# Kernel optimization log

Hardware: AMD Instinct MI355X
Metric: run time of the kernel (lower is better)

Reference implementation:

```python
import jax, jax.numpy as jnp
import numpy as np

S = 2048        # tokens (single prefill sequence)
HID = 3584      # hidden_size
H = 16          # num query heads
KV = 8          # num kv heads
D = 256         # head_dim
WINDOW = 1024   # sliding window size
CAP = 50.0      # logit softcap
SCALE = 256.0 ** -0.5   # query_pre_attn_scalar ** -0.5
THETA = 10000.0


def setup_inputs() -> dict:
    key = jax.random.key(0)
    ks = jax.random.split(key, 5)
    hidden_states = jax.random.normal(ks[0], (S, HID), dtype=jnp.float32)
    positions = jnp.arange(S, dtype=jnp.int32)
    Wq = jax.random.normal(ks[1], (HID, H * D), dtype=jnp.float32) * 0.02
    Wk = jax.random.normal(ks[2], (HID, KV * D), dtype=jnp.float32) * 0.02
    Wv = jax.random.normal(ks[3], (HID, KV * D), dtype=jnp.float32) * 0.02
    Wo = jax.random.normal(ks[4], (H * D, HID), dtype=jnp.float32) * 0.02
    return {"hidden_states": hidden_states, "positions": positions,
            "Wq": Wq, "Wk": Wk, "Wv": Wv, "Wo": Wo}


def _rope_neox(x, positions):
    # x: [S, n_heads, D]; neox-style: rotate halves, full rotary_dim == D
    half = D // 2
    inv_freq = 1.0 / (THETA ** (jnp.arange(0, half, dtype=jnp.float32) * 2.0 / D))
    freqs = positions.astype(jnp.float32)[:, None] * inv_freq[None, :]  # [S, half]
    cos = jnp.cos(freqs)[:, None, :].astype(x.dtype)
    sin = jnp.sin(freqs)[:, None, :].astype(x.dtype)
    x1, x2 = x[..., :half], x[..., half:]
    return jnp.concatenate([x1 * cos - x2 * sin, x2 * cos + x1 * sin], axis=-1)


def reference(hidden_states, positions, Wq, Wk, Wv, Wo):
    # QKV projections (no bias)
    q = (hidden_states @ Wq).reshape(S, H, D)
    k = (hidden_states @ Wk).reshape(S, KV, D)
    v = (hidden_states @ Wv).reshape(S, KV, D)
    q = _rope_neox(q, positions)
    k = _rope_neox(k, positions)
    # grouped-query attention: G query heads per kv head
    G = H // KV
    qg = q.reshape(S, KV, G, D)
    scores = jnp.einsum('qkgd,skd->kgqs', qg, k) * jnp.asarray(SCALE, q.dtype)
    # logit soft-capping
    scores = CAP * jnp.tanh(scores / CAP)
    # causal + sliding-window mask
    i = positions[:, None]
    j = positions[None, :]
    mask = (j <= i) & ((i - j) < WINDOW)   # [S, S]
    neg = jnp.finfo(scores.dtype).min
    scores = jnp.where(mask[None, None, :, :], scores, neg)
    p = jax.nn.softmax(scores, axis=-1)
    attn = jnp.einsum('kgqs,skd->qkgd', p, v).reshape(S, H * D)
    return attn @ Wo
```

## Files before the change

### kernel.cpp

```cpp
#include <hip/hip_runtime.h>
#include <stdint.h>

#define S 2048
#define HID 3584
#define NH 16
#define NKV 8
#define DH 256
#define WINDOW 1024
#define SCALE 0.0625f
#define CAP 50.0f

typedef short s16x8 __attribute__((ext_vector_type(8)));
typedef float f32x4 __attribute__((ext_vector_type(4)));

__device__ __forceinline__ short f2bf(float f) {
  union { float f; uint32_t u; } c; c.f = f;
  uint32_t u = c.u;
  uint32_t r = (u + 0x7FFFu + ((u >> 16) & 1u)) >> 16;
  return (short)r;
}
__device__ __forceinline__ float bf2f(short s) {
  union { uint32_t u; float f; } c;
  c.u = ((uint32_t)(uint16_t)s) << 16;
  return c.f;
}
__device__ __forceinline__ void gll16(const void* g, void* l) {
  __builtin_amdgcn_global_load_lds((const __attribute__((address_space(1))) void*)g,
                                   (__attribute__((address_space(3))) void*)l, 16, 0, 0);
}

__global__ void rope_table_kernel(float2* __restrict__ tbl) {
  int idx = blockIdx.x * 256 + threadIdx.x;
  int s = idx >> 7, i = idx & 127;
  float inv = __expf(-(float)i * (9.210340371976184f / 128.0f));
  float fr = (float)s * inv;
  tbl[idx] = make_float2(cosf(fr), sinf(fr));
}

__global__ void conv_hs_kernel(const float* __restrict__ src, short* __restrict__ dst) {
  int gid = blockIdx.x * 256 + threadIdx.x;
  float4 a = *(const float4*)&src[(size_t)gid * 8];
  float4 b = *(const float4*)&src[(size_t)gid * 8 + 4];
  s16x8 o;
  o[0] = f2bf(a.x); o[1] = f2bf(a.y); o[2] = f2bf(a.z); o[3] = f2bf(a.w);
  o[4] = f2bf(b.x); o[5] = f2bf(b.y); o[6] = f2bf(b.z); o[7] = f2bf(b.w);
  *(s16x8*)&dst[(size_t)gid * 8] = o;
}

__global__ __launch_bounds__(256)
void transpose_all_kernel(const float* __restrict__ Wq, const float* __restrict__ Wk,
                          const float* __restrict__ Wv, const float* __restrict__ Wo,
                          short* __restrict__ Wt, short* __restrict__ WtO)
{
  __shared__ __align__(16) short t[64][76];
  int b = blockIdx.x;
  const float* src; short* dst; int K, N, lb;
  if (b < 3584)      { src = Wq; dst = Wt;                       K = HID;  N = 4096; lb = b; }
  else if (b < 5376) { src = Wk; dst = Wt + (size_t)4096 * HID;  K = HID;  N = 2048; lb = b - 3584; }
  else if (b < 7168) { src = Wv; dst = Wt + (size_t)6144 * HID;  K = HID;  N = 2048; lb = b - 5376; }
  else               { src = Wo; dst = WtO;                      K = 4096; N = HID;  lb = b - 7168; }
  int ntn = N >> 6;
  int tn = lb % ntn, tk = lb / ntn;
  int tid = threadIdx.x;
  int c = tid & 63, rg = tid >> 6;
  #pragma unroll
  for (int i = 0; i < 4; ++i) {
    int r0 = i * 16 + rg * 4;
    short tmp[4];
    #pragma unroll
    for (int j = 0; j < 4; ++j)
      tmp[j] = f2bf(src[(size_t)(tk * 64 + r0 + j) * N + tn * 64 + c]);
    *(short4*)&t[c][r0] = *(short4*)tmp;
  }
  __syncthreads();
  #pragma unroll
  for (int it = 0; it < 2; ++it) {
    int flat = it * 256 + tid;
    int n = flat >> 3, kc = flat & 7;
    *(s16x8*)&dst[(size_t)(tn * 64 + n) * K + tk * 64 + kc * 8] = *(s16x8*)&t[n][kc * 8];
  }
}

__global__ __launch_bounds__(256)
void transpose_v_kernel(const short* __restrict__ vsb, short* __restrict__ vtb)
{
  __shared__ short t[64][74];
  int b = blockIdx.x;
  int kv = b >> 7;
  int rem = b & 127;
  int s0 = (rem >> 2) * 64, d0 = (rem & 3) * 64;
  const short* src = vsb + ((size_t)kv * S + s0) * DH + d0;
  short* dst = vtb + ((size_t)kv * DH + d0) * S + s0;
  int tid = threadIdx.x;
  int c = tid & 63, sb = (tid >> 6) * 16;
  #pragma unroll
  for (int ss = 0; ss < 16; ++ss)
    t[c][sb + ss] = src[(size_t)(sb + ss) * DH + c];
  __syncthreads();
  #pragma unroll
  for (int it = 0; it < 2; ++it) {
    int flat = it * 256 + tid;
    int r = flat >> 3, cc = (flat & 7) * 8;
    *(s16x8*)&dst[(size_t)r * S + cc] = *(s16x8*)&t[r][cc];
  }
}

__global__ __launch_bounds__(256, 2)
void qkv_gemm_kernel(const short* __restrict__ hsb, const short* __restrict__ Wt,
                     short* __restrict__ qb, short* __restrict__ kbuf,
                     short* __restrict__ vsb)
{
  __shared__ __align__(16) short Asb[256 * 64];
  __shared__ __align__(16) short Bsb[128 * 64];
  int bid = blockIdx.x;
  int i = bid >> 3;
  int bm = i & 7;
  int bn = (bid & 7) * 8 + (i >> 3);
  int m0 = bm * 256, n0 = bn * 128;
  int tid = threadIdx.x, w = tid >> 6, lane = tid & 63;
  int lr = lane & 15, lk = lane >> 4;
  int wm = (w >> 1) * 128, wn = (w & 1) * 64;
  int r7 = lr & 7;
  int abase = (wm + lr) * 64 + ((lk ^ r7) * 8);
  int bbase = (wn + lr) * 64 + ((lk ^ r7) * 8);
  int row8 = tid >> 3;
  int colsw = ((tid & 7) ^ (row8 & 7)) * 8;
  const short* srcA = hsb + (size_t)(m0 + row8) * HID + colsw;
  const short* srcB = Wt + (size_t)(n0 + row8) * HID + colsw;
  f32x4 acc[8][4] = {};
  for (int t = 0; t < HID / 64; ++t) {
    const short* sa = srcA + t * 64;
    const short* sb = srcB + t * 64;
    #pragma unroll
    for (int r = 0; r < 8; ++r)
      gll16(sa + (size_t)(r * 32) * HID, Asb + r * 2048 + w * 512);
    #pragma unroll
    for (int r = 0; r < 4; ++r)
      gll16(sb + (size_t)(r * 32) * HID, Bsb + r * 2048 + w * 512);
    __syncthreads();
    s16x8 bf[4][2];
    #pragma unroll
    for (int nf = 0; nf < 4; ++nf)
      #pragma unroll
      for (int kh = 0; kh < 2; ++kh)
        bf[nf][kh] = *(const s16x8*)&Bsb[(bbase + nf * 16 * 64) ^ (kh * 32)];
    #pragma unroll
    for (int mh = 0; mh < 2; ++mh) {
      s16x8 af[4][2];
      #pragma unroll
      for (int mf = 0; mf < 4; ++mf)
        #pragma unroll
        for (int kh = 0; kh < 2; ++kh)
          af[mf][kh] = *(const s16x8*)&Asb[(abase + (mh * 64 + mf * 16) * 64) ^ (kh * 32)];
      __builtin_amdgcn_s_setprio(1);
      #pragma unroll
      for (int mf = 0; mf < 4; ++mf)
        #pragma unroll
        for (int nf = 0; nf < 4; ++nf) {
          acc[mh * 4 + mf][nf] = __builtin_amdgcn_mfma_f32_16x16x32_bf16(
              af[mf][0], bf[nf][0], acc[mh * 4 + mf][nf], 0, 0, 0);
          acc[mh * 4 + mf][nf] = __builtin_amdgcn_mfma_f32_16x16x32_bf16(
              af[mf][1], bf[nf][1], acc[mh * 4 + mf][nf], 0, 0, 0);
        }
      __builtin_amdgcn_s_setprio(0);
    }
    __syncthreads();
  }
  int region = (n0 < 4096) ? 0 : ((n0 < 6144) ? 1 : 2);
  #pragma unroll
  for (int m = 0; m < 8; ++m) {
    int srow_b = m0 + wm + m * 16 + lk * 4;
    #pragma unroll
    for (int n = 0; n < 4; ++n) {
      int ncol = n0 + wn + n * 16 + lr;
      #pragma unroll
      for (int r = 0; r < 4; ++r) {
        int srow = srow_b + r;
        short bv = f2bf(acc[m][n][r]);
        if (region == 0) {
          int h = ncol >> 8, d = ncol & 255;
          qb[((size_t)h * S + srow) * DH + d] = bv;
        } else if (region == 1) {
          int c = ncol - 4096; int kv = c >> 8, d = c & 255;
          kbuf[((size_t)kv * S + srow) * DH + d] = bv;
        } else {
          int c = ncol - 6144; int kv = c >> 8, d = c & 255;
          vsb[((size_t)kv * S + srow) * DH + d] = bv;
        }
      }
    }
  }
}

__global__ __launch_bounds__(256)
void out_gemm_kernel(const short* __restrict__ attnb, const short* __restrict__ WtO,
                     float* __restrict__ out)
{
  __shared__ __align__(16) short Asb[128 * 64];
  __shared__ __align__(16) short Bsb[128 * 64];
  int bid = blockIdx.x;
  int flat = (bid & 7) * 56 + (bid >> 3);
  int bn = flat >> 4, bm = flat & 15;
  int m0 = bm * 128, n0 = bn * 128;
  int tid = threadIdx.x, w = tid >> 6, lane = tid & 63;
  int lr = lane & 15, lk = lane >> 4;
  int wm = (w >> 1) * 64, wn = (w & 1) * 64;
  int r7 = lr & 7;
  int abase = (wm + lr) * 64 + ((lk ^ r7) * 8);
  int bbase = (wn + lr) * 64 + ((lk ^ r7) * 8);
  int row8 = tid >> 3;
  int colsw = ((tid & 7) ^ (row8 & 7)) * 8;
  const short* srcA = attnb + (size_t)(m0 + row8) * 4096 + colsw;
  const short* srcB = WtO + (size_t)(n0 + row8) * 4096 + colsw;
  f32x4 acc[4][4] = {};
  for (int t = 0; t < 4096 / 64; ++t) {
    const short* sa = srcA + t * 64;
    const short* sb = srcB + t * 64;
    #pragma unroll
    for (int r = 0; r < 4; ++r)
      gll16(sa + (size_t)(r * 32) * 4096, Asb + r * 2048 + w * 512);
    #pragma unroll
    for (int r = 0; r < 4; ++r)
      gll16(sb + (size_t)(r * 32) * 4096, Bsb + r * 2048 + w * 512);
    __syncthreads();
    s16x8 af[4][2], bf[4][2];
    #pragma unroll
    for (int f = 0; f < 4; ++f)
      #pragma unroll
      for (int kh = 0; kh < 2; ++kh) {
        af[f][kh] = *(const s16x8*)&Asb[(abase + f * 16 * 64) ^ (kh * 32)];
        bf[f][kh] = *(const s16x8*)&Bsb[(bbase + f * 16 * 64) ^ (kh * 32)];
      }
    __builtin_amdgcn_s_setprio(1);
    #pragma unroll
    for (int mf = 0; mf < 4; ++mf)
      #pragma unroll
      for (int nf = 0; nf < 4; ++nf) {
        acc[mf][nf] = __builtin_amdgcn_mfma_f32_16x16x32_bf16(
            af[mf][0], bf[nf][0], acc[mf][nf], 0, 0, 0);
        acc[mf][nf] = __builtin_amdgcn_mfma_f32_16x16x32_bf16(
            af[mf][1], bf[nf][1], acc[mf][nf], 0, 0, 0);
      }
    __builtin_amdgcn_s_setprio(0);
    __syncthreads();
  }
  #pragma unroll
  for (int mf = 0; mf < 4; ++mf) {
    int srow_b = m0 + wm + mf * 16 + lk * 4;
    #pragma unroll
    for (int nf = 0; nf < 4; ++nf) {
      int ncol = n0 + wn + nf * 16 + lr;
      #pragma unroll
      for (int r = 0; r < 4; ++r)
        out[(size_t)(srow_b + r) * HID + ncol] = acc[mf][nf][r];
    }
  }
}

__global__ void rope_k_kernel(short* __restrict__ kbuf, const float2* __restrict__ tbl)
{
  int gid = blockIdx.x * 256 + threadIdx.x;
  int row = gid >> 4, ch = gid & 15;
  short* base = kbuf + (size_t)row * DH;
  int s = row & (S - 1);
  int i0 = ch * 8;
  s16x8 x1 = *(s16x8*)(base + i0);
  s16x8 x2 = *(s16x8*)(base + 128 + i0);
  s16x8 y1, y2;
  #pragma unroll
  for (int j = 0; j < 8; ++j) {
    float2 cs = tbl[s * 128 + i0 + j];
    float a = bf2f(x1[j]), b = bf2f(x2[j]);
    y1[j] = f2bf(a * cs.x - b * cs.y);
    y2[j] = f2bf(b * cs.x + a * cs.y);
  }
  *(s16x8*)(base + i0) = y1;
  *(s16x8*)(base + 128 + i0) = y2;
}

__global__ __launch_bounds__(512)
void attn_kernel(const short* __restrict__ qb, const short* __restrict__ kbuf,
                 const short* __restrict__ vtb, short* __restrict__ attnb,
                 const float2* __restrict__ tbl)
{
  __shared__ __align__(16) short Klds[2][64][256];
  __shared__ __align__(16) short Vlds[2][256][64];
  __shared__ __align__(16) short Plds[8][16][72];
  int bid = blockIdx.x;
  int qt = 31 - (bid >> 4), h = bid & 15;
  int kv = h >> 1;
  int q0 = qt * 64;
  int tid = threadIdx.x;
  int w = tid >> 6, lane = tid & 63;
  int g = w >> 2, wsub = w & 3;
  int gtid = tid & 255;
  int lr = lane & 15, lk = lane >> 4;
  int qrow_base = q0 + wsub * 16;
  s16x8 qf[8];
  {
    s16x8 qraw[8];
    const short* qrow = qb + ((size_t)h * S + (qrow_base + lr)) * DH;
    #pragma unroll
    for (int kb = 0; kb < 8; ++kb)
      qraw[kb] = *(const s16x8*)(qrow + kb * 32 + lk * 8);
    const float2* trow = tbl + (size_t)(qrow_base + lr) * 128 + lk * 8;
    #pragma unroll
    for (int kb = 0; kb < 4; ++kb)
      #pragma unroll
      for (int j = 0; j < 8; ++j) {
        float2 cs = trow[kb * 32 + j];
        float a = bf2f(qraw[kb][j]), b = bf2f(qraw[kb + 4][j]);
        qf[kb][j]     = f2bf(a * cs.x - b * cs.y);
        qf[kb + 4][j] = f2bf(b * cs.x + a * cs.y);
      }
  }
  f32x4 acc_o[16] = {};
  float l_r[4] = {0.0f, 0.0f, 0.0f, 0.0f};
  int tlo = (q0 >= WINDOW - 1) ? ((q0 - (WINDOW - 1)) >> 6) : 0;
  int thi = q0 >> 6;
  const short* kbase = kbuf + (size_t)kv * S * DH;
  const short* vbase = vtb + (size_t)kv * DH * S;

  s16x8 kpf[8], vpf[8];
  auto loadRegs = [&](int t) {
    int k0 = t * 64;
    #pragma unroll
    for (int it = 0; it < 8; ++it) {
      int flat = it * 256 + gtid;
      int r = flat >> 5, cg = flat & 31;
      kpf[it] = *(const s16x8*)(kbase + (size_t)(k0 + r) * DH + cg * 8);
    }
    #pragma unroll
    for (int it = 0; it < 8; ++it) {
      int flat = it * 256 + gtid;
      int r = flat >> 3, cg = flat & 7;
      vpf[it] = *(const s16x8*)(vbase + (size_t)r * S + k0 + cg * 8);
    }
  };
  auto writeLds = [&]() {
    #pragma unroll
    for (int it = 0; it < 8; ++it) {
      int flat = it * 256 + gtid;
      int r = flat >> 5, cg = flat & 31;
      *(s16x8*)&Klds[g][r][(cg ^ (r & 7)) * 8] = kpf[it];
    }
    #pragma unroll
    for (int it = 0; it < 8; ++it) {
      int flat = it * 256 + gtid;
      int r = flat >> 3, cg = flat & 7;
      *(s16x8*)&Vlds[g][r][(cg ^ (r & 7)) * 8] = vpf[it];
    }
  };

  int tg0 = tlo + g;
  int n_all = thi - tlo + 1;
  int jmax = (n_all + 1) >> 1;
  if (tg0 <= thi) loadRegs(tg0);
  for (int j = 0; j < jmax; ++j) {
    int t = tg0 + 2 * j;
    bool active = (t <= thi);
    if (active) writeLds();
    __syncthreads();
    if (active && t + 2 <= thi) loadRegs(t + 2);
    if (active) {
      int k0 = t * 64;
      f32x4 sc4[4] = {};
      __builtin_amdgcn_s_setprio(1);
      #pragma unroll
      for (int kb = 0; kb < 8; ++kb)
        #pragma unroll
        for (int ni = 0; ni < 4; ++ni) {
          int row = ni * 16 + lr;
          s16x8 b = *(const s16x8*)&Klds[g][row][(((kb << 2) | lk) ^ (row & 7)) * 8];
          sc4[ni] = __builtin_amdgcn_mfma_f32_16x16x32_bf16(qf[kb], b, sc4[ni], 0, 0, 0);
        }
      __builtin_amdgcn_s_setprio(0);
      bool interior = (k0 + 63 <= qrow_base) && (qrow_base + 15 - k0 < WINDOW);
      #pragma unroll
      for (int ni = 0; ni < 4; ++ni)
        #pragma unroll
        for (int r = 0; r < 4; ++r) {
          float raw = sc4[ni][r];
          float e2t = __expf(raw * (2.0f * SCALE / CAP));
          float p = __expf(__fdividef(-2.0f * CAP, 1.0f + e2t));
          if (!interior) {
            int qg = qrow_base + lk * 4 + r;
            int kg = k0 + ni * 16 + lr;
            bool valid = (kg <= qg) && (qg - kg < WINDOW);
            p = valid ? p : 0.0f;
          }
          sc4[ni][r] = p;
          l_r[r] += p;
        }
      #pragma unroll
      for (int ni = 0; ni < 4; ++ni)
        #pragma unroll
        for (int r = 0; r < 4; ++r)
          Plds[w][lk * 4 + r][ni * 16 + lr] = f2bf(sc4[ni][r]);
      s16x8 pa0 = *(const s16x8*)&Plds[w][lr][lk * 8];
      s16x8 pa1 = *(const s16x8*)&Plds[w][lr][32 + lk * 8];
      __builtin_amdgcn_s_setprio(1);
      #pragma unroll
      for (int df = 0; df < 16; ++df) {
        int row = df * 16 + lr;
        s16x8 b0 = *(const s16x8*)&Vlds[g][row][((lk ^ (row & 7)) * 8)];
        s16x8 b1 = *(const s16x8*)&Vlds[g][row][(((4 + lk) ^ (row & 7)) * 8)];
        acc_o[df] = __builtin_amdgcn_mfma_f32_16x16x32_bf16(pa0, b0, acc_o[df], 0, 0, 0);
        acc_o[df] = __builtin_amdgcn_mfma_f32_16x16x32_bf16(pa1, b1, acc_o[df], 0, 0, 0);
      }
      __builtin_amdgcn_s_setprio(0);
    }
    __syncthreads();
  }
  float lsum[4];
  #pragma unroll
  for (int r = 0; r < 4; ++r) {
    float v = l_r[r];
    #pragma unroll
    for (int off = 1; off < 16; off <<= 1)
      v += __shfl_xor(v, off, 64);
    lsum[r] = v;
  }
  float* comb = (float*)&Klds[0][0][0];
  float* lcomb = (float*)&Vlds[0][0][0];
  if (g == 1) {
    #pragma unroll
    for (int df = 0; df < 16; ++df)
      #pragma unroll
      for (int r = 0; r < 4; ++r)
        comb[(size_t)(wsub * 16 + lk * 4 + r) * 256 + df * 16 + lr] = acc_o[df][r];
    if (lr == 0)
      #pragma unroll
      for (int r = 0; r < 4; ++r)
        lcomb[wsub * 16 + lk * 4 + r] = lsum[r];
  }
  __syncthreads();
  if (g == 0) {
    #pragma unroll
    for (int r = 0; r < 4; ++r) {
      int rowi = wsub * 16 + lk * 4 + r;
      float lt = lsum[r] + lcomb[rowi];
      float inv = 1.0f / lt;
      int srow = q0 + rowi;
      #pragma unroll
      for (int df = 0; df < 16; ++df) {
        float o = acc_o[df][r] + comb[(size_t)rowi * 256 + df * 16 + lr];
        attnb[(size_t)srow * (NH * DH) + h * DH + df * 16 + lr] = f2bf(o * inv);
      }
    }
  }
}

extern "C" void kernel_launch(void* const* d_in, const int* in_sizes, int n_in,
                              void* d_out, int out_size, void* d_ws, size_t ws_size,
                              hipStream_t stream) {
  const float* hs = (const float*)d_in[0];
  const float* Wq = (const float*)d_in[2];
  const float* Wk = (const float*)d_in[3];
  const float* Wv = (const float*)d_in[4];
  const float* Wo = (const float*)d_in[5];
  float* out = (float*)d_out;
  char* ws = (char*)d_ws;
  size_t off = 0;
  float2* tbl  = (float2*)(ws + off); off += 2097152;
  short* qb    = (short*)(ws + off);  off += 16777216;
  short* kbuf  = (short*)(ws + off);  off += 8388608;
  short* vtb   = (short*)(ws + off);  off += 8388608;
  short* attnb = (short*)(ws + off);  off += 16777216;
  short* hsb   = (short*)(ws + off);  off += 14680064;
  short* Wt    = (short*)(ws + off);  off += 58720256;
  short* WtO   = (short*)(ws + off);  off += 29360128;
  short* vsb   = (short*)(ws + off);  off += 8388608;

  hipLaunchKernelGGL(rope_table_kernel, dim3(1024), dim3(256), 0, stream, tbl);
  hipLaunchKernelGGL(conv_hs_kernel, dim3(3584), dim3(256), 0, stream, hs, hsb);
  hipLaunchKernelGGL(transpose_all_kernel, dim3(10752), dim3(256), 0, stream,
                     Wq, Wk, Wv, Wo, Wt, WtO);
  hipLaunchKernelGGL(qkv_gemm_kernel, dim3(512), dim3(256), 0, stream,
                     hsb, Wt, qb, kbuf, vsb);
  hipLaunchKernelGGL(transpose_v_kernel, dim3(1024), dim3(256), 0, stream,
                     vsb, vtb);
  hipLaunchKernelGGL(rope_k_kernel, dim3(1024), dim3(256), 0, stream, kbuf, tbl);
  hipLaunchKernelGGL(attn_kernel, dim3(512), dim3(512), 0, stream,
                     qb, kbuf, vtb, attnb, tbl);
  hipLaunchKernelGGL(out_gemm_kernel, dim3(448), dim3(256), 0, stream,
                     attnb, WtO, out);
}
```

Baseline: 367.3 us.

## Halve attention KV tile, stage V directly to LDS, raise occupancy

The KV tile shrinks from 64 to 32 keys, so the K/V/P shared-memory buffers and the register prefetch arrays are roughly halved, and the launch bounds now request more resident waves. V is copied straight from global memory into LDS with a direct-load helper instead of going through registers, and an extra barrier separates that copy from the PV MFMAs. The final cross-group combine runs in two passes to fit the smaller LDS. The aim is higher occupancy and less register pressure, at the cost of twice as many loop iterations and barriers, with less MFMA work per barrier.

New measurement: 474.8 us. 29.3% more time.

```diff
diff --git a/kernel.cpp b/kernel.cpp
--- a/kernel.cpp
+++ b/kernel.cpp
@@ -278,14 +278,14 @@
   *(s16x8*)(base + 128 + i0) = y2;
 }
 
-__global__ __launch_bounds__(512)
+__global__ __launch_bounds__(512, 4)
 void attn_kernel(const short* __restrict__ qb, const short* __restrict__ kbuf,
                  const short* __restrict__ vtb, short* __restrict__ attnb,
                  const float2* __restrict__ tbl)
 {
-  __shared__ __align__(16) short Klds[2][64][256];
-  __shared__ __align__(16) short Vlds[2][256][64];
-  __shared__ __align__(16) short Plds[8][16][72];
+  __shared__ __align__(16) short Klds[2][32][256];
+  __shared__ __align__(16) short Vlds[2][256][32];
+  __shared__ __align__(16) short Plds[8][16][36];
   int bid = blockIdx.x;
   int qt = 31 - (bid >> 4), h = bid & 15;
   int kv = h >> 1;
@@ -316,68 +316,71 @@
   }
   f32x4 acc_o[16] = {};
   float l_r[4] = {0.0f, 0.0f, 0.0f, 0.0f};
-  int tlo = (q0 >= WINDOW - 1) ? ((q0 - (WINDOW - 1)) >> 6) : 0;
-  int thi = q0 >> 6;
+  int tlo = (q0 >= WINDOW - 1) ? ((q0 - (WINDOW - 1)) >> 5) : 0;
+  int thi = (q0 + 63) >> 5;
   const short* kbase = kbuf + (size_t)kv * S * DH;
   const short* vbase = vtb + (size_t)kv * DH * S;
 
-  s16x8 kpf[8], vpf[8];
-  auto loadRegs = [&](int t) {
-    int k0 = t * 64;
-    #pragma unroll
-    for (int it = 0; it < 8; ++it) {
+  s16x8 kpf[4];
+  auto loadK = [&](int t) {
+    int k0 = t * 32;
+    #pragma unroll
+    for (int it = 0; it < 4; ++it) {
       int flat = it * 256 + gtid;
       int r = flat >> 5, cg = flat & 31;
       kpf[it] = *(const s16x8*)(kbase + (size_t)(k0 + r) * DH + cg * 8);
     }
-    #pragma unroll
-    for (int it = 0; it < 8; ++it) {
-      int flat = it * 256 + gtid;
-      int r = flat >> 3, cg = flat & 7;
-      vpf[it] = *(const s16x8*)(vbase + (size_t)r * S + k0 + cg * 8);
-    }
   };
-  auto writeLds = [&]() {
-    #pragma unroll
-    for (int it = 0; it < 8; ++it) {
+  auto writeK = [&]() {
+    #pragma unroll
+    for (int it = 0; it < 4; ++it) {
       int flat = it * 256 + gtid;
       int r = flat >> 5, cg = flat & 31;
       *(s16x8*)&Klds[g][r][(cg ^ (r & 7)) * 8] = kpf[it];
     }
-    #pragma unroll
-    for (int it = 0; it < 8; ++it) {
+  };
+  auto stageV = [&](int t) {
+    int k0 = t * 32;
+    short* vg = (short*)&Vlds[g][0][0];
+    #pragma unroll
+    for (int it = 0; it < 4; ++it) {
       int flat = it * 256 + gtid;
-      int r = flat >> 3, cg = flat & 7;
-      *(s16x8*)&Vlds[g][r][(cg ^ (r & 7)) * 8] = vpf[it];
+      int r = flat >> 2, cg = flat & 3;
+      gll16(vbase + (size_t)r * S + k0 + ((cg ^ (r & 3)) * 8),
+            vg + it * 2048 + (gtid & ~63) * 8);
     }
   };
 
   int tg0 = tlo + g;
   int n_all = thi - tlo + 1;
   int jmax = (n_all + 1) >> 1;
-  if (tg0 <= thi) loadRegs(tg0);
+  if (tg0 <= thi) loadK(tg0);
   for (int j = 0; j < jmax; ++j) {
     int t = tg0 + 2 * j;
     bool active = (t <= thi);
-    if (active) writeLds();
-    __syncthreads();
-    if (active && t + 2 <= thi) loadRegs(t + 2);
+    int k0 = t * 32;
+    if (active) writeK();
+    __syncthreads();
     if (active) {
-      int k0 = t * 64;
-      f32x4 sc4[4] = {};
+      stageV(t);
+      if (t + 2 <= thi) loadK(t + 2);
+    }
+    s16x8 pa0;
+    if (active) {
+      f32x4 sc4[2] = {};
       __builtin_amdgcn_s_setprio(1);
       #pragma unroll
       for (int kb = 0; kb < 8; ++kb)
         #pragma unroll
-        for (int ni = 0; ni < 4; ++ni) {
+        for (int ni = 0; ni < 2; ++ni) {
           int row = ni * 16 + lr;
           s16x8 b = *(const s16x8*)&Klds[g][row][(((kb << 2) | lk) ^ (row & 7)) * 8];
           sc4[ni] = __builtin_amdgcn_mfma_f32_16x16x32_bf16(qf[kb], b, sc4[ni], 0, 0, 0);
         }
       __builtin_amdgcn_s_setprio(0);
-      bool interior = (k0 + 63 <= qrow_base) && (qrow_base + 15 - k0 < WINDOW);
-      #pragma unroll
-      for (int ni = 0; ni < 4; ++ni)
+      bool interior = (k0 + 31 <= qrow_base) && (qrow_base + 15 - k0 < WINDOW);
+      #pragma unroll
+      for (int ni = 0; ni < 2; ++ni)
         #pragma unroll
         for (int r = 0; r < 4; ++r) {
           float raw = sc4[ni][r];
@@ -393,24 +396,23 @@
           l_r[r] += p;
         }
       #pragma unroll
-      for (int ni = 0; ni < 4; ++ni)
+      for (int ni = 0; ni < 2; ++ni)
         #pragma unroll
         for (int r = 0; r < 4; ++r)
           Plds[w][lk * 4 + r][ni * 16 + lr] = f2bf(sc4[ni][r]);
-      s16x8 pa0 = *(const s16x8*)&Plds[w][lr][lk * 8];
-      s16x8 pa1 = *(const s16x8*)&Plds[w][lr][32 + lk * 8];
+      pa0 = *(const s16x8*)&Plds[w][lr][lk * 8];
+    }
+    __syncthreads();
+    if (active) {
       __builtin_amdgcn_s_setprio(1);
       #pragma unroll
       for (int df = 0; df < 16; ++df) {
         int row = df * 16 + lr;
-        s16x8 b0 = *(const s16x8*)&Vlds[g][row][((lk ^ (row & 7)) * 8)];
-        s16x8 b1 = *(const s16x8*)&Vlds[g][row][(((4 + lk) ^ (row & 7)) * 8)];
+        s16x8 b0 = *(const s16x8*)&Vlds[g][row][((lk ^ (row & 3))) * 8];
         acc_o[df] = __builtin_amdgcn_mfma_f32_16x16x32_bf16(pa0, b0, acc_o[df], 0, 0, 0);
-        acc_o[df] = __builtin_amdgcn_mfma_f32_16x16x32_bf16(pa1, b1, acc_o[df], 0, 0, 0);
       }
       __builtin_amdgcn_s_setprio(0);
     }
-    __syncthreads();
   }
   float lsum[4];
   #pragma unroll
@@ -421,31 +423,37 @@
       v += __shfl_xor(v, off, 64);
     lsum[r] = v;
   }
+  __syncthreads();
+  float* lcomb = (float*)&Plds[0][0][0];
+  if (g == 1 && lr == 0) {
+    #pragma unroll
+    for (int r = 0; r < 4; ++r)
+      lcomb[wsub * 16 + lk * 4 + r] = lsum[r];
+  }
   float* comb = (float*)&Klds[0][0][0];
-  float* lcomb = (float*)&Vlds[0][0][0];
-  if (g == 1) {
-    #pragma unroll
-    for (int df = 0; df < 16; ++df)
-      #pragma unroll
-      for (int r = 0; r < 4; ++r)
-        comb[(size_t)(wsub * 16 + lk * 4 + r) * 256 + df * 16 + lr] = acc_o[df][r];
-    if (lr == 0)
-      #pragma unroll
-      for (int r = 0; r < 4; ++r)
-        lcomb[wsub * 16 + lk * 4 + r] = lsum[r];
-  }
-  __syncthreads();
-  if (g == 0) {
-    #pragma unroll
-    for (int r = 0; r < 4; ++r) {
-      int rowi = wsub * 16 + lk * 4 + r;
-      float lt = lsum[r] + lcomb[rowi];
-      float inv = 1.0f / lt;
-      int srow = q0 + rowi;
-      #pragma unroll
-      for (int df = 0; df < 16; ++df) {
-        float o = acc_o[df][r] + comb[(size_t)rowi * 256 + df * 16 + lr];
-        attnb[(size_t)srow * (NH * DH) + h * DH + df * 16 + lr] = f2bf(o * inv);
+  #pragma unroll
+  for (int pass = 0; pass < 2; ++pass) {
+    __syncthreads();
+    if (g == 1) {
+      #pragma unroll
+      for (int df = 0; df < 8; ++df)
+        #pragma unroll
+        for (int r = 0; r < 4; ++r)
+          comb[(size_t)(wsub * 16 + lk * 4 + r) * 128 + df * 16 + lr] = acc_o[pass * 8 + df][r];
+    }
+    __syncthreads();
+    if (g == 0) {
+      #pragma unroll
+      for (int r = 0; r < 4; ++r) {
+        int rowi = wsub * 16 + lk * 4 + r;
+        float lt = lsum[r] + lcomb[rowi];
+        float inv = 1.0f / lt;
+        int srow = q0 + rowi;
+        #pragma unroll
+        for (int df = 0; df < 8; ++df) {
+          float o = acc_o[pass * 8 + df][r] + comb[(size_t)rowi * 128 + df * 16 + lr];
+          attnb[(size_t)srow * (NH * DH) + h * DH + (pass * 8 + df) * 16 + lr] = f2bf(o * inv);
+        }
       }
     }
   }
```
